# Kernel tuning notes

Measured on AMD Instinct MI355X. Metric: run time of the kernel, lower is better.

Reference implementation:

```python
import jax, jax.numpy as jnp
import numpy as np

B = 16            # batch of graphs
N = 512           # n_node
D = 32            # embedding_dim
MAXN = 16         # max_neighbors
E = MAXN * (N - 1)   # 8176 edges per graph
SLEFT = N * D
FSS = 601         # full_support_size
NA = N - 1        # num_actions (so one-hot rows == B*n_node)
IN0 = D + 1       # sa feature dim
NTOT = B * N


def _gat(x, snd, rcv, W, a_src, a_dst, b):
    # single-head GATConv, add_self_loops=False
    h = x @ W                                            # [BN, C]
    e = (h * a_src).sum(-1)[snd] + (h * a_dst).sum(-1)[rcv]
    e = jnp.where(e > 0, e, 0.2 * e)                     # LeakyReLU(0.2)
    m = jax.ops.segment_max(e, rcv, num_segments=NTOT)   # segment softmax
    m = jnp.where(jnp.isfinite(m), m, 0.0)
    ee = jnp.exp(e - m[rcv])
    den = jax.ops.segment_sum(ee, rcv, num_segments=NTOT)
    alpha = ee / (den[rcv] + 1e-16)
    return jax.ops.segment_sum(alpha[:, None] * h[snd], rcv, num_segments=NTOT) + b


def _ln(x, s, o):
    # hk.LayerNorm(axis=-2): normalize over node axis, scale/offset over features
    x3 = x.reshape(B, N, -1)
    mu = x3.mean(axis=1, keepdims=True)
    var = ((x3 - mu) ** 2).mean(axis=1, keepdims=True)
    return ((x3 - mu) * jax.lax.rsqrt(var + 1e-5) * s + o).reshape(B * N, -1)


def _gat_params(key, din, dout):
    k1, k2, k3 = jax.random.split(key, 3)
    sc = 1.0 / np.sqrt(din)
    return (jax.random.normal(k1, (din, dout), jnp.float32) * sc,
            jax.random.normal(k2, (dout,), jnp.float32) * sc,
            jax.random.normal(k3, (dout,), jnp.float32) * sc,
            jnp.zeros((dout,), jnp.float32))


def setup_inputs():
    key = jax.random.key(0)
    ks = jax.random.split(key, 4)
    nodes = jax.random.normal(ks[0], (B, SLEFT), jnp.float32)
    snd = jax.random.randint(ks[1], (B, E), 0, N).astype(jnp.float32)
    rcv = jax.random.randint(ks[2], (B, E), 0, N).astype(jnp.float32)
    ns = jnp.concatenate([nodes, snd, rcv], axis=1)      # [B, SLEFT + 2E]
    a = jax.random.randint(ks[3], (B,), 0, NA + 1)
    inp = {"ns": ns, "a": a}
    dims = [(IN0, 4 * D), (4 * D, 2 * D), (2 * D, 2 * D), (2 * D, D)]
    rdims = [(IN0, FSS), (FSS, FSS), (FSS, FSS), (FSS, FSS)]
    for i, (di, do) in enumerate(dims, 1):
        W, asrc, adst, b = _gat_params(jax.random.fold_in(key, 100 + i), di, do)
        inp.update({f"W{i}": W, f"a{i}s": asrc, f"a{i}d": adst, f"b{i}": b})
        if i < 4:
            inp.update({f"s{i}": jnp.ones((do,), jnp.float32), f"o{i}": jnp.zeros((do,), jnp.float32)})
    for i, (di, do) in enumerate(rdims, 1):
        W, asrc, adst, b = _gat_params(jax.random.fold_in(key, 200 + i), di, do)
        inp.update({f"rW{i}": W, f"ra{i}s": asrc, f"ra{i}d": adst, f"rb{i}": b})
        if i < 4:
            inp.update({f"rs{i}": jnp.ones((FSS,), jnp.float32), f"ro{i}": jnp.zeros((FSS,), jnp.float32)})
    return inp


def reference(ns, a,
              W1, a1s, a1d, b1, s1, o1,
              W2, a2s, a2d, b2, s2, o2,
              W3, a3s, a3d, b3, s3, o3,
              W4, a4s, a4d, b4,
              rW1, ra1s, ra1d, rb1, rs1, ro1,
              rW2, ra2s, ra2d, rb2, rs2, ro2,
              rW3, ra3s, ra3d, rb3, rs3, ro3,
              rW4, ra4s, ra4d, rb4):
    # gbatch: offset per-graph indices into one big graph
    off = (jnp.arange(B, dtype=jnp.int32) * N)[:, None]
    snd = (ns[:, SLEFT:SLEFT + E].astype(jnp.int32) + off).reshape(-1)
    rcv = (ns[:, SLEFT + E:SLEFT + 2 * E].astype(jnp.int32) + off).reshape(-1)
    nodes = ns[:, :SLEFT].reshape(B * N, D)
    sa = jnp.concatenate([nodes, jax.nn.one_hot(a, NA + 1).reshape(-1, 1)], axis=1)
    # reward head
    r = jax.nn.relu(_ln(_gat(sa, snd, rcv, rW1, ra1s, ra1d, rb1), rs1, ro1))
    r = jax.nn.relu(_ln(_gat(r, snd, rcv, rW2, ra2s, ra2d, rb2), rs2, ro2))
    r = jax.nn.relu(_ln(_gat(r, snd, rcv, rW3, ra3s, ra3d, rb3), rs3, ro3))
    r = _gat(r, snd, rcv, rW4, ra4s, ra4d, rb4).reshape(B, N, FSS).sum(axis=1)
    # next-state head
    f = jax.nn.relu(_ln(_gat(sa, snd, rcv, W1, a1s, a1d, b1), s1, o1))
    f = jax.nn.relu(_ln(_gat(f, snd, rcv, W2, a2s, a2d, b2), s2, o2))
    f = jax.nn.relu(_ln(_gat(f, snd, rcv, W3, a3s, a3d, b3), s3, o3))
    f = _gat(f, snd, rcv, W4, a4s, a4d, b4).reshape(B, N * D)
    ns_new = jnp.concatenate([f, ns[:, SLEFT:]], axis=1)
    return (r, ns_new)
```

## Files before the change

kernel.cpp:

```cpp
#include <hip/hip_runtime.h>
#include <math.h>

#define B_ 16
#define N_ 512
#define D_ 32
#define E_ 8176
#define SLEFT_ 16384
#define FSS_ 601
#define BN_ (B_*N_)
#define BE_ (B_*E_)
#define NSROW_ (SLEFT_ + 2*E_)
#define OUT_R_ (B_*FSS_)
#define HLD_ 768
#define CAP_ 128

typedef __attribute__((ext_vector_type(8))) short short8;
typedef __attribute__((ext_vector_type(4))) float f32x4;

typedef __attribute__((address_space(3))) uint lds_uint;
typedef __attribute__((address_space(1))) const uint g_uint;

__device__ __forceinline__ void gl_lds16(const ushort* gp, ushort* lp) {
  __builtin_amdgcn_global_load_lds((g_uint*)gp, (lds_uint*)lp, 16, 0, 0);
}

__device__ __forceinline__ ushort f2b(float f) {
  uint u = __builtin_bit_cast(uint, f);
  u += 0x7FFFu + ((u >> 16) & 1u);
  return (ushort)(u >> 16);
}
__device__ __forceinline__ float b2f(ushort h) {
  return __builtin_bit_cast(float, ((uint)h) << 16);
}


struct SetupP {
  const float* ns; const int* a;
  int* cnt; int* bins; ushort* sa;
  const float* Wr[4]; const float* Wn[4]; ushort* T[4];
};

__global__ __launch_bounds__(256) void k_setup(SetupP p) {
  __shared__ float tile[32][33];
  int blk = blockIdx.x;
  if (blk < 511) {
    int idx = blk*256 + threadIdx.x;
    if (idx >= BE_) return;
    int b = idx / E_;
    int j = idx - b*E_;
    const float* row = p.ns + (size_t)b*NSROW_;
    int s = (int)row[SLEFT_ + j];
    int r = (int)row[SLEFT_ + E_ + j];
    int dst = b*N_ + r;
    int pos = atomicAdd(&p.cnt[dst], 1);
    if (pos < CAP_) p.bins[(size_t)dst*CAP_ + pos] = b*N_ + s;
    return;
  }
  if (blk < 2559) {
    int idx = (blk-511)*256 + threadIdx.x;
    int v = idx >> 6, c = idx & 63;
    int b = v >> 9, n = v & 511;
    float val = 0.f;
    if (c < 32)       val = p.ns[(size_t)b*NSROW_ + n*32 + c];
    else if (c == 32) val = (p.a[b]==n) ? 1.f : 0.f;
    p.sa[idx] = f2b(val);
    return;
  }
  int t = blk - 2559;
  int s, base, KP, DINR, DINN, DOUTN, KOFF;
  if (t < 48)        { s=0; base=0;    KP=64;  DINR=33;  DINN=33;  DOUTN=128; KOFF=0;   }
  else if (t < 600)  { s=1; base=48;   KP=736; DINR=601; DINN=128; DOUTN=64;  KOFF=608; }
  else if (t < 1104) { s=2; base=600;  KP=672; DINR=601; DINN=64;  DOUTN=64;  KOFF=608; }
  else               { s=3; base=1104; KP=672; DINR=601; DINN=64;  DOUTN=32;  KOFF=608; }
  int ti = t - base;
  int kt = ti / 24, nt = ti - kt*24;
  int k0 = kt*32, n0 = nt*32;
  int tid = threadIdx.x;
  int cc = tid & 31, rr = tid >> 5;
  #pragma unroll
  for (int it=0; it<4; it++) {
    int k = k0 + it*8 + rr;
    int n = n0 + cc;
    float v = 0.f;
    if (n < 640) { if (n < 601 && k < DINR) v = p.Wr[s][(size_t)k*601 + n]; }
    else { int nn = n-640, kk = k-KOFF;
           if (nn < DOUTN && kk >= 0 && kk < DINN) v = p.Wn[s][(size_t)kk*DOUTN + nn]; }
    tile[it*8+rr][cc] = v;
  }
  __syncthreads();
  #pragma unroll
  for (int it=0; it<4; it++) {
    int n = n0 + it*8 + rr;
    int k = k0 + cc;
    p.T[s][(size_t)n*KP + k] = f2b(tile[cc][it*8+rr]);
  }
}


__global__ __launch_bounds__(256) void k_gemm(const ushort* __restrict__ A,
                                              const ushort* __restrict__ Bt,
                                              ushort* __restrict__ C,
                                              float* __restrict__ esed,
                                              const float* __restrict__ asr,
                                              const float* __restrict__ adr,
                                              const float* __restrict__ asn,
                                              const float* __restrict__ adn,
                                              int Kpad, int dn,
                                              int kRewEnd, int kNextBeg) {
  __shared__ ushort Asm[64*32];
  __shared__ ushort Bsm[128*32];
  int tid = threadIdx.x;
  int rowBase = blockIdx.y * 64;
  int colBase = blockIdx.x * 128;
  int kBeg = (blockIdx.x == 5) ? kNextBeg : 0;
  int kEnd = (blockIdx.x == 5) ? Kpad : kRewEnd;
  int wave = tid >> 6, lane = tid & 63;
  int wr = (wave >> 1) * 32, wc = (wave & 1) * 64;
  int lm = lane & 15, lk = (lane >> 4) * 8;

  f32x4 acc[2][4];
  #pragma unroll
  for (int i=0;i<2;i++)
    #pragma unroll
    for (int j=0;j<4;j++) acc[i][j] = (f32x4){0.f,0.f,0.f,0.f};

  int t0 = tid, t1 = tid + 256;
  const ushort* Ag0 = A  + (size_t)(rowBase + (t0>>2))*Kpad + (t0&3)*8;
  const ushort* Bg0 = Bt + (size_t)(colBase + (t0>>2))*Kpad + (t0&3)*8;
  const ushort* Bg1 = Bt + (size_t)(colBase + (t1>>2))*Kpad + (t1&3)*8;
  ushort* Al0 = &Asm[t0*8];
  ushort* Bl0 = &Bsm[t0*8];
  ushort* Bl1 = &Bsm[t1*8];

  for (int k0 = kBeg; k0 < kEnd; k0 += 32) {
    gl_lds16(Ag0 + k0, Al0);
    gl_lds16(Bg0 + k0, Bl0);
    gl_lds16(Bg1 + k0, Bl1);
    __syncthreads();
    short8 af[2], bfr[4];
    #pragma unroll
    for (int i=0;i<2;i++) af[i]  = *(short8*)&Asm[(wr + i*16 + lm)*32 + lk];
    #pragma unroll
    for (int j=0;j<4;j++) bfr[j] = *(short8*)&Bsm[(wc + j*16 + lm)*32 + lk];
    #pragma unroll
    for (int i=0;i<2;i++)
      #pragma unroll
      for (int j=0;j<4;j++)
        acc[i][j] = __builtin_amdgcn_mfma_f32_16x16x32_bf16(af[i], bfr[j], acc[i][j], 0,0,0);
    __syncthreads();
  }

  float asv[4], adv[4];
  #pragma unroll
  for (int j=0;j<4;j++) {
    int col = colBase + wc + j*16 + lm;
    float s = 0.f, d = 0.f;
    if (col < 601)      { s = asr[col];     d = adr[col]; }
    else if (col >= 640 && col - 640 < dn) { s = asn[col-640]; d = adn[col-640]; }
    asv[j] = s; adv[j] = d;
  }
  int cr = lane >> 4;
  int ct2 = blockIdx.x*2 + (wc >> 6);
  float* esp = (ct2 < 10) ? esed : esed + 2*BN_;
  #pragma unroll
  for (int i=0;i<2;i++) {
    #pragma unroll
    for (int j=0;j<4;j++) {
      int col = colBase + wc + j*16 + lm;
      #pragma unroll
      for (int g=0; g<4; g++) {
        int row = rowBase + wr + i*16 + cr*4 + g;
        C[(size_t)row*HLD_ + col] = f2b(acc[i][j][g]);
      }
    }
    #pragma unroll
    for (int g=0; g<4; g++) {
      float se = 0.f, sd = 0.f;
      #pragma unroll
      for (int j=0;j<4;j++) { se += acc[i][j][g]*asv[j]; sd += acc[i][j][g]*adv[j]; }
      #pragma unroll
      for (int o=1;o<16;o<<=1) { se += __shfl_xor(se,o,64); sd += __shfl_xor(sd,o,64); }
      if (lm == 0) {
        int row = rowBase + wr + i*16 + cr*4 + g;
        atomicAdd(&esp[row], se);
        atomicAdd(&esp[BN_ + row], sd);
      }
    }
  }
}


__global__ __launch_bounds__(256) void k_agg(const ushort* __restrict__ h,
                                             const float* __restrict__ esed,
                                             const int* __restrict__ cnt,
                                             const int* __restrict__ bins,
                                             const float* __restrict__ bias_r,
                                             const float* __restrict__ bias_n,
                                             ushort* __restrict__ g,
                                             int dn) {
  const float* es_r = esed;
  const float* ed_r = esed + BN_;
  const float* es_n = esed + 2*BN_;
  const float* ed_n = esed + 3*BN_;
  int wid = threadIdx.x>>6, lane = threadIdx.x&63;
  int bid = blockIdx.x;
  int xcd = bid & 7, slot = bid >> 3;
  int graph = xcd + ((slot >> 7) << 3);
  int v = graph*512 + (slot & 127)*4 + wid;
  int s0 = v * CAP_;
  int deg = cnt[v]; if (deg > CAP_) deg = CAP_;
  float edr = ed_r[v], edn = ed_n[v];

  int ch0 = lane, ch1 = lane + 64;
  bool a1 = ch1 < 96;
  bool c1r = ch1 < 80;
  float acc0[8], acc1[8];
  #pragma unroll
  for (int q=0;q<8;q++){ acc0[q]=0.f; acc1[q]=0.f; }

  if (deg <= 64) {
    bool has = lane < deg;
    int u = 0; float er = -__builtin_inff(), en = -__builtin_inff();
    if (has) {
      u = bins[s0 + lane];
      er = es_r[u] + edr; er = er > 0.f ? er : 0.2f*er;
      en = es_n[u] + edn; en = en > 0.f ? en : 0.2f*en;
    }
    float mr = er, mn = en;
    #pragma unroll
    for (int o=32;o;o>>=1) { mr = fmaxf(mr, __shfl_xor(mr,o,64)); mn = fmaxf(mn, __shfl_xor(mn,o,64)); }
    float pr = has ? __expf(er - mr) : 0.f;
    float pn = has ? __expf(en - mn) : 0.f;
    float dr = pr, dnm = pn;
    #pragma unroll
    for (int o=32;o;o>>=1) { dr += __shfl_xor(dr,o,64); dnm += __shfl_xor(dnm,o,64); }
    pr *= 1.f/(dr + 1e-16f);
    pn *= 1.f/(dnm + 1e-16f);

    for (int t0 = 0; t0 < deg; t0 += 4) {
      int nt = deg - t0; if (nt > 4) nt = 4;
      short8 va[4], vb[4];
      float w0[4], w1[4];
      #pragma unroll
      for (int q=0;q<4;q++) {
        if (q < nt) {
          int uu = __shfl(u, t0+q, 64);
          w0[q] = __shfl(pr, t0+q, 64);
          w1[q] = __shfl(pn, t0+q, 64);
          const ushort* hp = h + (size_t)uu*HLD_;
          va[q] = *(const short8*)&hp[ch0*8];
          vb[q] = a1 ? *(const short8*)&hp[ch1*8] : short8{};
        } else {
          w0[q] = 0.f; w1[q] = 0.f; va[q] = short8{}; vb[q] = short8{};
        }
      }
      #pragma unroll
      for (int q=0;q<4;q++) {
        #pragma unroll
        for (int r=0;r<8;r++) acc0[r] += w0[q] * b2f((ushort)va[q][r]);
        if (a1) {
          float wv = c1r ? w0[q] : w1[q];
          #pragma unroll
          for (int r=0;r<8;r++) acc1[r] += wv * b2f((ushort)vb[q][r]);
        }
      }
    }
  } else {
    int e0 = s0 + deg;
    float mr = -__builtin_inff(), mn = -__builtin_inff();
    for (int j = s0 + lane; j < e0; j += 64) {
      int u = bins[j];
      float er = es_r[u] + edr; er = er>0.f?er:0.2f*er;
      float en = es_n[u] + edn; en = en>0.f?en:0.2f*en;
      mr = fmaxf(mr, er); mn = fmaxf(mn, en);
    }
    #pragma unroll
    for (int o=32;o;o>>=1) { mr=fmaxf(mr,__shfl_xor(mr,o,64)); mn=fmaxf(mn,__shfl_xor(mn,o,64)); }
    float dr=0.f, dnm=0.f;
    for (int j = s0 + lane; j < e0; j += 64) {
      int u = bins[j];
      float er = es_r[u] + edr; er = er>0.f?er:0.2f*er;
      float en = es_n[u] + edn; en = en>0.f?en:0.2f*en;
      dr += __expf(er-mr); dnm += __expf(en-mn);
    }
    #pragma unroll
    for (int o=32;o;o>>=1) { dr+=__shfl_xor(dr,o,64); dnm+=__shfl_xor(dnm,o,64); }
    float ir = 1.f/(dr+1e-16f), in_ = 1.f/(dnm+1e-16f);
    for (int j = s0; j < e0; ++j) {
      int uu = bins[j];
      float er = es_r[uu] + edr; er = er>0.f?er:0.2f*er;
      float en = es_n[uu] + edn; en = en>0.f?en:0.2f*en;
      float wr2 = __expf(er-mr)*ir, wn2 = __expf(en-mn)*in_;
      const ushort* hp = h + (size_t)uu*HLD_;
      short8 hv = *(const short8*)&hp[ch0*8];
      #pragma unroll
      for (int q=0;q<8;q++) acc0[q] += wr2 * b2f((ushort)hv[q]);
      if (a1) {
        short8 hv2 = *(const short8*)&hp[ch1*8];
        float wv = c1r ? wr2 : wn2;
        #pragma unroll
        for (int q=0;q<8;q++) acc1[q] += wv * b2f((ushort)hv2[q]);
      }
    }
  }

  ushort* gv = g + (size_t)v*HLD_;
  {
    int cb = ch0*8;
    short8 ov;
    #pragma unroll
    for (int q=0;q<8;q++) ov[q] = (short)f2b(acc0[q] + bias_r[cb+q]);
    *(short8*)&gv[cb] = ov;
  }
  if (a1) {
    int cb = ch1*8;
    short8 ov;
    #pragma unroll
    for (int q=0;q<8;q++) {
      int c = cb+q;
      float val;
      if (c < 601)                         val = acc1[q] + bias_r[c];
      else if (c >= 640 && (c-640) < dn)   val = acc1[q] + bias_n[c-640];
      else                                 val = 0.f;
      ov[q] = (short)f2b(val);
    }
    *(short8*)&gv[cb] = ov;
  }
}


__global__ __launch_bounds__(256) void k_ln_stats(const ushort* __restrict__ g,
                                                  float* __restrict__ st) {
  int b = blockIdx.y, z = blockIdx.z; int n0 = z*128;
  int lc = threadIdx.x & 63, r0 = threadIdx.x >> 6;
  int c = blockIdx.x*64 + lc;
  float s=0.f, q=0.f;
  #pragma unroll 4
  for (int i=0;i<32;i++) {
    int n = n0 + r0*32 + i;
    float x = b2f(g[(size_t)(b*N_+n)*HLD_ + c]);
    s+=x; q+=x*x;
  }
  __shared__ float S[4][64], Q[4][64];
  S[r0][lc]=s; Q[r0][lc]=q; __syncthreads();
  if (r0==0) {
    st[((size_t)(z*2+0)*B_ + b)*HLD_ + c] = S[0][lc]+S[1][lc]+S[2][lc]+S[3][lc];
    st[((size_t)(z*2+1)*B_ + b)*HLD_ + c] = Q[0][lc]+Q[1][lc]+Q[2][lc]+Q[3][lc];
  }
}


__global__ __launch_bounds__(256) void k_ln_apply(const ushort* __restrict__ g,
                                                  const float* __restrict__ st,
                                                  const float* __restrict__ scr,
                                                  const float* __restrict__ ofr,
                                                  const float* __restrict__ scn,
                                                  const float* __restrict__ ofn,
                                                  ushort* __restrict__ xb,
                                                  int dn, int Kpad) {
  int tid = threadIdx.x;
  int pp = blockIdx.x*128 + (tid & 127);
  int c0 = pp*2;
  if (c0 >= Kpad) return;
  int vbase = blockIdx.y*16;
  int b = vbase >> 9;
  float mv[2], av[2];
  #pragma unroll
  for (int q=0;q<2;q++) {
    int c = c0+q;
    int cs; bool valid; float scale, offs;
    if (c < 608) { cs = c; valid = c < 601;
                   scale = valid ? scr[c] : 0.f; offs = valid ? ofr[c] : 0.f; }
    else { int cn = c - 608; cs = 640 + cn; valid = cn < dn;
           scale = valid ? scn[cn] : 0.f; offs = valid ? ofn[cn] : 0.f; }
    float mul = 0.f, add = 0.f;
    if (valid) {
      float s=0.f, qq=0.f;
      #pragma unroll
      for (int z=0;z<4;z++) {
        s  += st[((size_t)(z*2+0)*B_ + b)*HLD_ + cs];
        qq += st[((size_t)(z*2+1)*B_ + b)*HLD_ + cs];
      }
      float mu = s*(1.f/N_);
      float var = qq*(1.f/N_) - mu*mu;
      float rs = rsqrtf(var+1e-5f);
      mul = rs*scale;
      add = offs - mu*rs*scale;
    }
    mv[q] = mul; av[q] = add;
  }
  int cs0 = (c0 < 608) ? c0 : 640 + (c0 - 608);
  for (int i = tid >> 7; i < 16; i += 2) {
    int v = vbase + i;
    uint gg = *(const uint*)&g[(size_t)v*HLD_ + cs0];
    float x0 = b2f((ushort)(gg & 0xFFFFu));
    float x1 = b2f((ushort)(gg >> 16));
    float y0 = x0*mv[0] + av[0]; y0 = y0 > 0.f ? y0 : 0.f;
    float y1 = x1*mv[1] + av[1]; y1 = y1 > 0.f ? y1 : 0.f;
    *(uint*)&xb[(size_t)v*Kpad + c0] = ((uint)f2b(y1) << 16) | f2b(y0);
  }
}


__global__ __launch_bounds__(256) void k_rsum(const ushort* __restrict__ g,
                                              float* __restrict__ rsp) {
  int b = blockIdx.y, z = blockIdx.z; int n0 = z*64;
  int lc = threadIdx.x & 63, r0 = threadIdx.x>>6;
  int c = blockIdx.x*64 + lc;
  float s = 0.f;
  if (c < FSS_) {
    #pragma unroll 4
    for (int i=0;i<16;i++) {
      int n = n0 + r0*16 + i;
      s += b2f(g[(size_t)(b*N_+n)*HLD_ + c]);
    }
  }
  __shared__ float S[4][64];
  S[r0][lc]=s; __syncthreads();
  if (r0==0 && c<FSS_)
    rsp[((size_t)z*B_ + b)*FSS_ + c] = S[0][lc]+S[1][lc]+S[2][lc]+S[3][lc];
}


__global__ __launch_bounds__(256) void k_final(const float* __restrict__ rsp,
                                               const ushort* __restrict__ g,
                                               const float* __restrict__ ns,
                                               float* __restrict__ out) {
  int idx = blockIdx.x*256+threadIdx.x;
  if (idx < OUT_R_) {
    int b = idx / FSS_, c = idx - b*FSS_;
    float s = 0.f;
    #pragma unroll
    for (int z=0;z<8;z++) s += rsp[((size_t)z*B_ + b)*FSS_ + c];
    out[idx] = s;
  } else {
    int j2 = idx - OUT_R_;
    if (j2 >= B_*NSROW_) return;
    int b = j2 / NSROW_; int j = j2 - b*NSROW_;
    float v;
    if (j < SLEFT_) {
      int n = j >> 5, c = j & 31;
      v = b2f(g[(size_t)(b*N_+n)*HLD_ + 640 + c]);
    } else {
      v = ns[(size_t)b*NSROW_ + j];
    }
    out[idx] = v;
  }
}


extern "C" void kernel_launch(void* const* d_in, const int* in_sizes, int n_in,
                              void* d_out, int out_size, void* d_ws, size_t ws_size,
                              hipStream_t stream) {
  const float* ns = (const float*)d_in[0];
  const int*   a  = (const int*)d_in[1];

  const float *W[4], *As[4], *Ad[4], *Bb[4], *Sc[3], *Of[3];
  const float *rW[4], *rAs[4], *rAd[4], *rBb[4], *rSc[3], *rOf[3];
  int p = 2;
  for (int i=0;i<4;i++){
    W[i]=(const float*)d_in[p++]; As[i]=(const float*)d_in[p++];
    Ad[i]=(const float*)d_in[p++]; Bb[i]=(const float*)d_in[p++];
    if (i<3){ Sc[i]=(const float*)d_in[p++]; Of[i]=(const float*)d_in[p++]; }
  }
  for (int i=0;i<4;i++){
    rW[i]=(const float*)d_in[p++]; rAs[i]=(const float*)d_in[p++];
    rAd[i]=(const float*)d_in[p++]; rBb[i]=(const float*)d_in[p++];
    if (i<3){ rSc[i]=(const float*)d_in[p++]; rOf[i]=(const float*)d_in[p++]; }
  }

  char* w = (char*)d_ws;
  auto carve = [&](size_t bytes)->void* {
    void* r = (void*)w;
    w += (bytes + 255) & ~(size_t)255;
    return r;
  };
  ushort* xb   = (ushort*)carve((size_t)BN_*736*2);
  ushort* hbuf = (ushort*)carve((size_t)BN_*HLD_*2);
  ushort* gbuf = (ushort*)carve((size_t)BN_*HLD_*2);
  ushort* sabf = (ushort*)carve((size_t)BN_*64*2);
  int* cnt     = (int*)carve((size_t)(BN_ + 4*4*BN_)*4);
  float* esedL = (float*)(cnt + BN_);
  int* bins    = (int*)carve((size_t)BN_*CAP_*4);
  float* stp   = (float*)carve((size_t)8*B_*HLD_*4);
  float* rsp   = (float*)carve((size_t)8*B_*FSS_*4);
  ushort* Wt[4];
  Wt[0] = (ushort*)carve((size_t)768*64*2);
  Wt[1] = (ushort*)carve((size_t)768*736*2);
  Wt[2] = (ushort*)carve((size_t)768*672*2);
  Wt[3] = (ushort*)carve((size_t)768*672*2);

  float* out = (float*)d_out;

  hipMemsetAsync(cnt, 0, (size_t)(BN_ + 16*BN_)*4, stream);

  SetupP sp;
  sp.ns = ns; sp.a = a; sp.cnt = cnt; sp.bins = bins; sp.sa = sabf;
  for (int i=0;i<4;i++){ sp.Wr[i]=rW[i]; sp.Wn[i]=W[i]; sp.T[i]=Wt[i]; }
  k_setup<<<4167, 256, 0, stream>>>(sp);

  dim3 ggrid(6, BN_/64);

  const ushort* xin[4] = { sabf, xb, xb, xb };
  int Kp[4]   = { 64, 736, 672, 672 };
  int dns[4]  = { 128, 64, 64, 32 };
  int kRe[4]  = { 64, 608, 608, 608 };
  int kNb[4]  = { 0, 608, 608, 608 };

  for (int L=0; L<4; ++L) {
    float* esed = esedL + (size_t)L*4*BN_;
    k_gemm<<<ggrid, 256, 0, stream>>>(xin[L], Wt[L], hbuf, esed,
                                      rAs[L], rAd[L], As[L], Ad[L], Kp[L], dns[L],
                                      kRe[L], kNb[L]);
    k_agg<<<BN_/4, 256, 0, stream>>>(hbuf, esed, cnt, bins,
                                     rBb[L], Bb[L], gbuf, dns[L]);
    if (L < 3) {
      k_ln_stats<<<dim3(12, B_, 4), 256, 0, stream>>>(gbuf, stp);
      int Kpn = (L==0) ? 736 : 672;
      k_ln_apply<<<dim3(3, BN_/16), 256, 0, stream>>>(gbuf, stp,
                  rSc[L], rOf[L], Sc[L], Of[L], xb, dns[L], Kpn);
    }
  }

  k_rsum<<<dim3(10, B_, 8), 256, 0, stream>>>(gbuf, rsp);
  k_final<<<(OUT_R_ + B_*NSROW_ + 255)/256, 256, 0, stream>>>(rsp, gbuf, ns, out);
}
```

Baseline: 366.0 us.

## Fuse LayerNorm apply and ReLU into GEMM A-tile load

Replaces the separate LayerNorm-apply kernel, which wrote a normalized bf16 activation buffer, with a small kernel that computes per-graph per-column scale/offset vectors. The GEMM then reads the raw aggregated buffer directly, applies scale, offset and ReLU in registers and stores the tile to LDS. This removes one full read/write pass over the activations per layer. In exchange the A tile now goes through registers instead of the direct global-to-LDS load, which adds per-element ALU work inside the GEMM loop. The aggregation kernel's channel bound is also changed to depend on dn.

New measurement: 354.2 us, median of 2. 3.2% less time.

```diff
diff --git a/kernel.cpp b/kernel.cpp
--- a/kernel.cpp
+++ b/kernel.cpp
@@ -13,6 +13,7 @@
 #define OUT_R_ (B_*FSS_)
 #define HLD_ 768
 #define CAP_ 128
+#define KXB_ 736
 
 typedef __attribute__((ext_vector_type(8))) short short8;
 typedef __attribute__((ext_vector_type(4))) float f32x4;
@@ -105,10 +106,13 @@
                                               const float* __restrict__ adr,
                                               const float* __restrict__ asn,
                                               const float* __restrict__ adn,
+                                              const float* __restrict__ mulb,
+                                              const float* __restrict__ addb,
                                               int Kpad, int dn,
-                                              int kRewEnd, int kNextBeg) {
+                                              int kRewEnd, int kNextBeg, int useLN) {
   __shared__ ushort Asm[64*32];
   __shared__ ushort Bsm[128*32];
+  __shared__ float Lm[KXB_], La[KXB_];
   int tid = threadIdx.x;
   int rowBase = blockIdx.y * 64;
   int colBase = blockIdx.x * 128;
@@ -125,17 +129,43 @@
     for (int j=0;j<4;j++) acc[i][j] = (f32x4){0.f,0.f,0.f,0.f};
 
   int t0 = tid, t1 = tid + 256;
-  const ushort* Ag0 = A  + (size_t)(rowBase + (t0>>2))*Kpad + (t0&3)*8;
+  int ar = t0 >> 2, ac8 = (t0 & 3) * 8;
   const ushort* Bg0 = Bt + (size_t)(colBase + (t0>>2))*Kpad + (t0&3)*8;
   const ushort* Bg1 = Bt + (size_t)(colBase + (t1>>2))*Kpad + (t1&3)*8;
-  ushort* Al0 = &Asm[t0*8];
   ushort* Bl0 = &Bsm[t0*8];
   ushort* Bl1 = &Bsm[t1*8];
+  ushort* Al0 = &Asm[t0*8];
+
+  const ushort* Ag_lds = A + (size_t)(rowBase + ar)*Kpad + ac8;
+  int koff = (blockIdx.x == 5) ? 32 : 0;
+  const ushort* Ag_vg  = A + (size_t)(rowBase + ar)*HLD_ + koff;
+
+  if (useLN) {
+    int b = rowBase >> 9;
+    for (int i = tid; i < KXB_; i += 256) {
+      Lm[i] = mulb[(size_t)b*KXB_ + i];
+      La[i] = addb[(size_t)b*KXB_ + i];
+    }
+    __syncthreads();
+  }
 
   for (int k0 = kBeg; k0 < kEnd; k0 += 32) {
-    gl_lds16(Ag0 + k0, Al0);
     gl_lds16(Bg0 + k0, Bl0);
     gl_lds16(Bg1 + k0, Bl1);
+    if (useLN) {
+      short8 av = *(const short8*)&Ag_vg[k0 + ac8];
+      short8 ov;
+      #pragma unroll
+      for (int q=0;q<8;q++) {
+        float x = b2f((ushort)av[q]);
+        float y = x * Lm[k0 + ac8 + q] + La[k0 + ac8 + q];
+        y = y > 0.f ? y : 0.f;
+        ov[q] = (short)f2b(y);
+      }
+      *(short8*)Al0 = ov;
+    } else {
+      gl_lds16(Ag_lds + k0, Al0);
+    }
     __syncthreads();
     short8 af[2], bfr[4];
     #pragma unroll
@@ -211,8 +241,9 @@
   int deg = cnt[v]; if (deg > CAP_) deg = CAP_;
   float edr = ed_r[v], edn = ed_n[v];
 
+  int nch = (640 + dn + 7) >> 3;
   int ch0 = lane, ch1 = lane + 64;
-  bool a1 = ch1 < 96;
+  bool a1 = ch1 < nch;
   bool c1r = ch1 < 80;
   float acc0[8], acc1[8];
   #pragma unroll
@@ -350,55 +381,38 @@
 }
 
 
-__global__ __launch_bounds__(256) void k_ln_apply(const ushort* __restrict__ g,
-                                                  const float* __restrict__ st,
-                                                  const float* __restrict__ scr,
-                                                  const float* __restrict__ ofr,
-                                                  const float* __restrict__ scn,
-                                                  const float* __restrict__ ofn,
-                                                  ushort* __restrict__ xb,
-                                                  int dn, int Kpad) {
-  int tid = threadIdx.x;
-  int pp = blockIdx.x*128 + (tid & 127);
-  int c0 = pp*2;
-  if (c0 >= Kpad) return;
-  int vbase = blockIdx.y*16;
-  int b = vbase >> 9;
-  float mv[2], av[2];
-  #pragma unroll
-  for (int q=0;q<2;q++) {
-    int c = c0+q;
-    int cs; bool valid; float scale, offs;
-    if (c < 608) { cs = c; valid = c < 601;
-                   scale = valid ? scr[c] : 0.f; offs = valid ? ofr[c] : 0.f; }
-    else { int cn = c - 608; cs = 640 + cn; valid = cn < dn;
-           scale = valid ? scn[cn] : 0.f; offs = valid ? ofn[cn] : 0.f; }
-    float mul = 0.f, add = 0.f;
-    if (valid) {
-      float s=0.f, qq=0.f;
-      #pragma unroll
-      for (int z=0;z<4;z++) {
-        s  += st[((size_t)(z*2+0)*B_ + b)*HLD_ + cs];
-        qq += st[((size_t)(z*2+1)*B_ + b)*HLD_ + cs];
-      }
-      float mu = s*(1.f/N_);
-      float var = qq*(1.f/N_) - mu*mu;
-      float rs = rsqrtf(var+1e-5f);
-      mul = rs*scale;
-      add = offs - mu*rs*scale;
-    }
-    mv[q] = mul; av[q] = add;
-  }
-  int cs0 = (c0 < 608) ? c0 : 640 + (c0 - 608);
-  for (int i = tid >> 7; i < 16; i += 2) {
-    int v = vbase + i;
-    uint gg = *(const uint*)&g[(size_t)v*HLD_ + cs0];
-    float x0 = b2f((ushort)(gg & 0xFFFFu));
-    float x1 = b2f((ushort)(gg >> 16));
-    float y0 = x0*mv[0] + av[0]; y0 = y0 > 0.f ? y0 : 0.f;
-    float y1 = x1*mv[1] + av[1]; y1 = y1 > 0.f ? y1 : 0.f;
-    *(uint*)&xb[(size_t)v*Kpad + c0] = ((uint)f2b(y1) << 16) | f2b(y0);
-  }
+__global__ __launch_bounds__(256) void k_stfin(const float* __restrict__ st,
+                                               const float* __restrict__ scr,
+                                               const float* __restrict__ ofr,
+                                               const float* __restrict__ scn,
+                                               const float* __restrict__ ofn,
+                                               float* __restrict__ mulb,
+                                               float* __restrict__ addb,
+                                               int dn) {
+  int c = blockIdx.x*256 + threadIdx.x;
+  int b = blockIdx.y;
+  if (c >= KXB_) return;
+  int cs; bool valid; float scale, offs;
+  if (c < 608) { cs = c; valid = c < 601;
+                 scale = valid ? scr[c] : 0.f; offs = valid ? ofr[c] : 0.f; }
+  else { int cn = c - 608; cs = 640 + cn; valid = cn < dn;
+         scale = valid ? scn[cn] : 0.f; offs = valid ? ofn[cn] : 0.f; }
+  float mul = 0.f, add = 0.f;
+  if (valid) {
+    float s=0.f, qq=0.f;
+    #pragma unroll
+    for (int z=0;z<4;z++) {
+      s  += st[((size_t)(z*2+0)*B_ + b)*HLD_ + cs];
+      qq += st[((size_t)(z*2+1)*B_ + b)*HLD_ + cs];
+    }
+    float mu = s*(1.f/N_);
+    float var = qq*(1.f/N_) - mu*mu;
+    float rs = rsqrtf(var+1e-5f);
+    mul = rs*scale;
+    add = offs - mu*rs*scale;
+  }
+  mulb[(size_t)b*KXB_ + c] = mul;
+  addb[(size_t)b*KXB_ + c] = add;
 }
 
 
@@ -475,7 +489,6 @@
     w += (bytes + 255) & ~(size_t)255;
     return r;
   };
-  ushort* xb   = (ushort*)carve((size_t)BN_*736*2);
   ushort* hbuf = (ushort*)carve((size_t)BN_*HLD_*2);
   ushort* gbuf = (ushort*)carve((size_t)BN_*HLD_*2);
   ushort* sabf = (ushort*)carve((size_t)BN_*64*2);
@@ -483,6 +496,8 @@
   float* esedL = (float*)(cnt + BN_);
   int* bins    = (int*)carve((size_t)BN_*CAP_*4);
   float* stp   = (float*)carve((size_t)8*B_*HLD_*4);
+  float* mulb  = (float*)carve((size_t)B_*KXB_*4);
+  float* addb  = (float*)carve((size_t)B_*KXB_*4);
   float* rsp   = (float*)carve((size_t)8*B_*FSS_*4);
   ushort* Wt[4];
   Wt[0] = (ushort*)carve((size_t)768*64*2);
@@ -501,7 +516,6 @@
 
   dim3 ggrid(6, BN_/64);
 
-  const ushort* xin[4] = { sabf, xb, xb, xb };
   int Kp[4]   = { 64, 736, 672, 672 };
   int dns[4]  = { 128, 64, 64, 32 };
   int kRe[4]  = { 64, 608, 608, 608 };
@@ -509,16 +523,17 @@
 
   for (int L=0; L<4; ++L) {
     float* esed = esedL + (size_t)L*4*BN_;
-    k_gemm<<<ggrid, 256, 0, stream>>>(xin[L], Wt[L], hbuf, esed,
-                                      rAs[L], rAd[L], As[L], Ad[L], Kp[L], dns[L],
-                                      kRe[L], kNb[L]);
+    const ushort* Ain = (L==0) ? sabf : gbuf;
+    k_gemm<<<ggrid, 256, 0, stream>>>(Ain, Wt[L], hbuf, esed,
+                                      rAs[L], rAd[L], As[L], Ad[L],
+                                      mulb, addb, Kp[L], dns[L],
+                                      kRe[L], kNb[L], (L==0)?0:1);
     k_agg<<<BN_/4, 256, 0, stream>>>(hbuf, esed, cnt, bins,
                                      rBb[L], Bb[L], gbuf, dns[L]);
     if (L < 3) {
       k_ln_stats<<<dim3(12, B_, 4), 256, 0, stream>>>(gbuf, stp);
-      int Kpn = (L==0) ? 736 : 672;
-      k_ln_apply<<<dim3(3, BN_/16), 256, 0, stream>>>(gbuf, stp,
-                  rSc[L], rOf[L], Sc[L], Of[L], xb, dns[L], Kpn);
+      k_stfin<<<dim3(3, B_), 256, 0, stream>>>(stp, rSc[L], rOf[L], Sc[L], Of[L],
+                                               mulb, addb, dns[L]);
     }
   }
 
```
